# Kernel optimization log

Measured on AMD Instinct MI355X. Metric: run time of the kernel, lower is better.

## Reference

```python
import jax, jax.numpy as jnp
import numpy as np
from jax import lax


def setup_inputs() -> dict:
    key = jax.random.key(0)
    ks = jax.random.split(key, 6)
    B, S, I, H = 64, 2048, 512, 512
    stdv = 1.0 / np.sqrt(H)
    return {
        "inputs": jax.random.normal(ks[0], (B, S, I), dtype=jnp.float32),
        "state": jax.random.normal(ks[1], (B, H), dtype=jnp.float32),
        "w_ih": jax.random.uniform(ks[2], (H, I), minval=-stdv, maxval=stdv, dtype=jnp.float32),
        "b_ih": jax.random.uniform(ks[3], (H, 1), minval=-stdv, maxval=stdv, dtype=jnp.float32),
        "w_hh": jax.random.uniform(ks[4], (H, H), minval=-stdv, maxval=stdv, dtype=jnp.float32),
        "b_hh": jax.random.uniform(ks[5], (H, 1), minval=-stdv, maxval=stdv, dtype=jnp.float32),
    }


def reference(inputs, state, w_ih, b_ih, w_hh, b_hh):
    """Tanh RNN: h_t = tanh(W_ih x_t + b_ih + W_hh h_{t-1} + b_hh).
    Returns (hidden_seq [S*B, H] (per-step states concatenated along dim 0,
    matching torch.cat(dim=0) in the original), h_last_T [H, B])."""
    B, S, I = inputs.shape
    H = w_hh.shape[0]
    # Hoist the input projection out of the recurrence: [B, S, H]
    x_proj = jnp.einsum('bsi,hi->bsh', inputs, w_ih) + (b_ih[:, 0] + b_hh[:, 0])

    def step(h, xp_t):  # h: [B, H], xp_t: [B, H]
        h_new = jnp.tanh(xp_t + h @ w_hh.T)
        return h_new, h_new

    h_last, hs = lax.scan(step, state, jnp.swapaxes(x_proj, 0, 1))  # hs: [S, B, H]
    hidden_seq = hs.reshape(S * B, H)
    return hidden_seq, h_last.T  # h_last.T matches the original's returned h_t of shape [H, B]
```

## Files before the change

kernel.cpp:

```cpp
#include <hip/hip_runtime.h>


typedef _Float16 half8 __attribute__((ext_vector_type(8)));
typedef _Float16 half4 __attribute__((ext_vector_type(4)));
typedef float f32x4 __attribute__((ext_vector_type(4)));
typedef unsigned long long u64;

#define S_SZ 2048
#define OUT1_OFF 67108864ull

#define XP_OFF    0ull
#define WHH_OFF   134217728ull
#define WIH_OFF   134742016ull
#define BIAS_OFF  135266304ull

#define WLDS_SZ   131072
#define HB_SZ     8192
#define SMEM_SZ   147456

__device__ __forceinline__ float fast_tanh(float x) {
    float a = exp2f(x * 2.8853900817779268f);
    return (a - 1.0f) * __builtin_amdgcn_rcpf(a + 1.0f);
}

__global__ void prep_kernel(const float* __restrict__ wih, const float* __restrict__ whh,
                            const float* __restrict__ bih, const float* __restrict__ bhh,
                            _Float16* __restrict__ wih16, _Float16* __restrict__ whh16,
                            float* __restrict__ bias)
{
    const int i = blockIdx.x * 256 + threadIdx.x;
    wih16[i] = (_Float16)wih[i];
    whh16[i] = (_Float16)whh[i];
    if (i < 512) bias[i] = bih[i] + bhh[i];
}

__global__ __launch_bounds__(512, 1) void xproj_kernel(
    const float* __restrict__ inputs, const _Float16* __restrict__ wih16,
    const float* __restrict__ bias, _Float16* __restrict__ xp16)
{
    __shared__ _Float16 Alds[64 * 512];
    const int s = blockIdx.x;

    for (int idx = threadIdx.x; idx < 64 * 128; idx += 512) {
        const int row = idx >> 7, chunk = idx & 127;
        const float4 v = *reinterpret_cast<const float4*>(
            inputs + ((size_t)row * S_SZ + s) * 512 + chunk * 4);
        half4 hv;
        hv[0] = (_Float16)v.x; hv[1] = (_Float16)v.y;
        hv[2] = (_Float16)v.z; hv[3] = (_Float16)v.w;
        const int bc = (chunk * 8) ^ ((row & 7) << 4);
        *reinterpret_cast<half4*>(reinterpret_cast<char*>(Alds) + row * 1024 + bc) = hv;
    }
    __syncthreads();

    const int lane = threadIdx.x & 63, w = threadIdx.x >> 6;
    const int l15 = lane & 15, lg = lane >> 4;

    f32x4 acc[4][4];
    #pragma unroll
    for (int m = 0; m < 4; ++m)
        #pragma unroll
        for (int n = 0; n < 4; ++n)
            acc[m][n] = 0.0f;

    for (int kk = 0; kk < 16; ++kk) {
        half8 af[4], bf[4];
        #pragma unroll
        for (int m = 0; m < 4; ++m) {
            const int row = m * 16 + l15;
            const int bc = (kk * 64 + lg * 16) ^ ((row & 7) << 4);
            af[m] = *reinterpret_cast<const half8*>(
                reinterpret_cast<const char*>(Alds) + row * 1024 + bc);
        }
        #pragma unroll
        for (int n = 0; n < 4; ++n) {
            const int col = w * 64 + n * 16 + l15;
            bf[n] = *reinterpret_cast<const half8*>(wih16 + (size_t)col * 512 + kk * 32 + lg * 8);
        }
        #pragma unroll
        for (int m = 0; m < 4; ++m)
            #pragma unroll
            for (int n = 0; n < 4; ++n)
                acc[m][n] = __builtin_amdgcn_mfma_f32_16x16x32_f16(bf[n], af[m], acc[m][n], 0, 0, 0);
    }

    #pragma unroll
    for (int m = 0; m < 4; ++m) {
        const int brow = m * 16 + l15;
        #pragma unroll
        for (int n = 0; n < 4; ++n) {
            const int j0 = w * 64 + n * 16 + lg * 4;
            const float4 bv = *reinterpret_cast<const float4*>(bias + j0);
            half4 hv;
            hv[0] = (_Float16)(acc[m][n][0] + bv.x);
            hv[1] = (_Float16)(acc[m][n][1] + bv.y);
            hv[2] = (_Float16)(acc[m][n][2] + bv.z);
            hv[3] = (_Float16)(acc[m][n][3] + bv.w);
            *reinterpret_cast<half4*>(xp16 + ((size_t)s * 64 + brow) * 512 + j0) = hv;
        }
    }
}

__global__ __launch_bounds__(256, 1) void rnn_step_kernel(
    const _Float16* __restrict__ whh16, const _Float16* __restrict__ xp16,
    const float* __restrict__ state, float* __restrict__ out)
{
    extern __shared__ __align__(16) char smem[];
    char* wlds = smem;
    char* hb   = smem + WLDS_SZ;

    const int r = blockIdx.x;
    const int tid = threadIdx.x;
    const int lane = tid & 63, w = tid >> 6;
    const int l15 = lane & 15, lg = lane >> 4;
    const int row8 = l15 & 7;
    const bool hi = (l15 >= 8);

    for (int idx = tid; idx < 16 * 512; idx += 256) {
        const int c = idx >> 9, jj = idx & 511;
        const int kk = 12 + (c >> 2), lgc = c & 3;
        *reinterpret_cast<half8*>(wlds + c * 8192 + jj * 16) =
            *reinterpret_cast<const half8*>(whh16 + (size_t)jj * 512 + kk * 32 + lgc * 8);
    }
    for (int idx = tid; idx < 512; idx += 256) {
        const int row = idx & 7, lgc = (idx >> 3) & 3, kk = idx >> 5;
        const float* sp = state + (size_t)(r * 8 + row) * 512 + kk * 32 + lgc * 8;
        const float4 v0 = *reinterpret_cast<const float4*>(sp);
        const float4 v1 = *reinterpret_cast<const float4*>(sp + 4);
        half8 hv;
        hv[0] = (_Float16)v0.x; hv[1] = (_Float16)v0.y;
        hv[2] = (_Float16)v0.z; hv[3] = (_Float16)v0.w;
        hv[4] = (_Float16)v1.x; hv[5] = (_Float16)v1.y;
        hv[6] = (_Float16)v1.z; hv[7] = (_Float16)v1.w;
        *reinterpret_cast<half8*>(hb + ((kk * 4 + lgc) * 8 + row) * 16) = hv;
    }

    half8 wa[64], wv[32];
    {
        const _Float16* wp = whh16 + (size_t)(w * 128 + l15) * 512 + lg * 8;
        #pragma unroll
        for (int jt = 0; jt < 8; ++jt) {
            #pragma unroll
            for (int kk = 0; kk < 8; ++kk)
                wa[jt * 8 + kk] = *reinterpret_cast<const half8*>(wp + jt * 16 * 512 + kk * 32);
            #pragma unroll
            for (int kk = 8; kk < 12; ++kk)
                wv[jt * 4 + kk - 8] = *reinterpret_cast<const half8*>(wp + jt * 16 * 512 + kk * 32);
        }
    }
    #pragma unroll
    for (int i = 0; i < 64; ++i) asm volatile("" : "+a"(wa[i]));
    #pragma unroll
    for (int i = 0; i < 32; ++i) asm volatile("" : "+v"(wv[i]));

    u64 xq[4];
    {
        const _Float16* xpb = xp16 + (size_t)(r * 8 + row8) * 512
                              + w * 128 + (hi ? 64 : 0) + lg * 4;
        #pragma unroll
        for (int i = 0; i < 4; ++i)
            xq[i] = *reinterpret_cast<const u64*>(xpb + i * 16);
    }

    __syncthreads();

    #pragma unroll 1
    for (int t = 0; t < S_SZ; ++t) {
        const char* hc = hb + (t & 1) * HB_SZ;
        char* hn = hb + ((t + 1) & 1) * HB_SZ;

        f32x4 acc[8];
        #pragma unroll
        for (int jt = 0; jt < 8; ++jt) acc[jt] = 0.0f;

        #pragma unroll
        for (int kk = 0; kk < 8; ++kk) {
            const half8 bf = *reinterpret_cast<const half8*>(
                hc + ((kk * 4 + lg) * 8 + row8) * 16);
            #pragma unroll
            for (int jt = 0; jt < 8; ++jt)
                acc[jt] = __builtin_amdgcn_mfma_f32_16x16x32_f16(
                    wa[jt * 8 + kk], bf, acc[jt], 0, 0, 0);
        }
        #pragma unroll
        for (int kk = 8; kk < 12; ++kk) {
            const half8 bf = *reinterpret_cast<const half8*>(
                hc + ((kk * 4 + lg) * 8 + row8) * 16);
            #pragma unroll
            for (int jt = 0; jt < 8; ++jt)
                acc[jt] = __builtin_amdgcn_mfma_f32_16x16x32_f16(
                    wv[jt * 4 + kk - 8], bf, acc[jt], 0, 0, 0);
        }
        #pragma unroll
        for (int kk = 12; kk < 16; ++kk) {
            const half8 bf = *reinterpret_cast<const half8*>(
                hc + ((kk * 4 + lg) * 8 + row8) * 16);
            const char* wc = wlds + ((kk - 12) * 4 + lg) * 8192;
            #pragma unroll
            for (int jt = 0; jt < 8; ++jt) {
                const half8 a = *reinterpret_cast<const half8*>(
                    wc + (w * 128 + jt * 16 + l15) * 16);
                acc[jt] = __builtin_amdgcn_mfma_f32_16x16x32_f16(a, bf, acc[jt], 0, 0, 0);
            }
        }

        const int rowi = r * 8 + row8;
        #pragma unroll
        for (int i = 0; i < 4; ++i) {
            const f32x4 a = hi ? acc[i + 4] : acc[i];
            union { _Float16 h[4]; u64 u; } xv, hp;
            xv.u = xq[i];
            f32x4 f;
            #pragma unroll
            for (int q = 0; q < 4; ++q) {
                f[q] = fast_tanh(a[q] + (float)xv.h[q]);
                hp.h[q] = (_Float16)f[q];
            }
            const int j0 = w * 128 + (hi ? 64 : 0) + i * 16 + lg * 4;
            const int e = (((j0 >> 5) * 4 + ((j0 >> 3) & 3)) * 8 + row8);
            *reinterpret_cast<u64*>(hn + e * 16 + (lg & 1) * 8) = hp.u;
            *reinterpret_cast<f32x4*>(out + ((size_t)t * 64 + rowi) * 512 + j0) = f;
            if (t == S_SZ - 1) {
                #pragma unroll
                for (int q = 0; q < 4; ++q)
                    out[OUT1_OFF + (size_t)(j0 + q) * 64 + rowi] = f[q];
            }
        }

        if (t + 1 < S_SZ) {
            const _Float16* xpb = xp16 + ((size_t)(t + 1) * 64 + rowi) * 512
                                  + w * 128 + (hi ? 64 : 0) + lg * 4;
            #pragma unroll
            for (int i = 0; i < 4; ++i)
                xq[i] = *reinterpret_cast<const u64*>(xpb + i * 16);
        }

        asm volatile("s_waitcnt lgkmcnt(0)" ::: "memory");
        __builtin_amdgcn_s_barrier();
    }
}

extern "C" void kernel_launch(void* const* d_in, const int* in_sizes, int n_in,
                              void* d_out, int out_size, void* d_ws, size_t ws_size,
                              hipStream_t stream)
{
    const float* inputs = (const float*)d_in[0];
    const float* state  = (const float*)d_in[1];
    const float* w_ih   = (const float*)d_in[2];
    const float* b_ih   = (const float*)d_in[3];
    const float* w_hh   = (const float*)d_in[4];
    const float* b_hh   = (const float*)d_in[5];
    float* out = (float*)d_out;
    char* ws = (char*)d_ws;

    _Float16* xp16  = (_Float16*)(ws + XP_OFF);
    _Float16* whh16 = (_Float16*)(ws + WHH_OFF);
    _Float16* wih16 = (_Float16*)(ws + WIH_OFF);
    float*    bias  = (float*)(ws + BIAS_OFF);

    hipFuncSetAttribute((const void*)rnn_step_kernel,
                        hipFuncAttributeMaxDynamicSharedMemorySize, SMEM_SZ);

    prep_kernel<<<1024, 256, 0, stream>>>(w_ih, w_hh, b_ih, b_hh, wih16, whh16, bias);
    xproj_kernel<<<S_SZ, 512, 0, stream>>>(inputs, wih16, bias, xp16);
    rnn_step_kernel<<<8, 256, SMEM_SZ, stream>>>(whh16, xp16, state, out);
}
```

Before: 6.852 ms.

## Split recurrent step across eight waves per block instead of four

Doubles the threads per recurrence block from 256 to 512. Each wave now owns 64 hidden columns instead of 128, which halves the per-wave MFMA chain, the register-resident weight slice and the epilogue work on every serial step. The register-resident weights are merged into a single AGPR array, and the h write offset is recomputed to match the new column mapping. In exchange there are more waves to synchronise at each step's barrier, and the launch bound of two blocks per CU does not match the 144KB LDS each block uses.

Result: slower. 8.523 ms (+24.4%).

```diff
diff --git a/kernel.cpp b/kernel.cpp
--- a/kernel.cpp
+++ b/kernel.cpp
@@ -101,7 +101,7 @@
     }
 }
 
-__global__ __launch_bounds__(256, 1) void rnn_step_kernel(
+__global__ __launch_bounds__(512, 2) void rnn_step_kernel(
     const _Float16* __restrict__ whh16, const _Float16* __restrict__ xp16,
     const float* __restrict__ state, float* __restrict__ out)
 {
@@ -116,13 +116,14 @@
     const int row8 = l15 & 7;
     const bool hi = (l15 >= 8);
 
-    for (int idx = tid; idx < 16 * 512; idx += 256) {
+    for (int idx = tid; idx < 16 * 512; idx += 512) {
         const int c = idx >> 9, jj = idx & 511;
         const int kk = 12 + (c >> 2), lgc = c & 3;
         *reinterpret_cast<half8*>(wlds + c * 8192 + jj * 16) =
             *reinterpret_cast<const half8*>(whh16 + (size_t)jj * 512 + kk * 32 + lgc * 8);
     }
-    for (int idx = tid; idx < 512; idx += 256) {
+    if (tid < 512) {
+        const int idx = tid;
         const int row = idx & 7, lgc = (idx >> 3) & 3, kk = idx >> 5;
         const float* sp = state + (size_t)(r * 8 + row) * 512 + kk * 32 + lgc * 8;
         const float4 v0 = *reinterpret_cast<const float4*>(sp);
@@ -135,31 +136,24 @@
         *reinterpret_cast<half8*>(hb + ((kk * 4 + lgc) * 8 + row) * 16) = hv;
     }
 
-    half8 wa[64], wv[32];
+    half8 wa[48];
     {
-        const _Float16* wp = whh16 + (size_t)(w * 128 + l15) * 512 + lg * 8;
-        #pragma unroll
-        for (int jt = 0; jt < 8; ++jt) {
-            #pragma unroll
-            for (int kk = 0; kk < 8; ++kk)
-                wa[jt * 8 + kk] = *reinterpret_cast<const half8*>(wp + jt * 16 * 512 + kk * 32);
-            #pragma unroll
-            for (int kk = 8; kk < 12; ++kk)
-                wv[jt * 4 + kk - 8] = *reinterpret_cast<const half8*>(wp + jt * 16 * 512 + kk * 32);
-        }
+        const _Float16* wp = whh16 + (size_t)(w * 64 + l15) * 512 + lg * 8;
+        #pragma unroll
+        for (int jt = 0; jt < 4; ++jt)
+            #pragma unroll
+            for (int kk = 0; kk < 12; ++kk)
+                wa[jt * 12 + kk] = *reinterpret_cast<const half8*>(wp + jt * 16 * 512 + kk * 32);
     }
     #pragma unroll
-    for (int i = 0; i < 64; ++i) asm volatile("" : "+a"(wa[i]));
-    #pragma unroll
-    for (int i = 0; i < 32; ++i) asm volatile("" : "+v"(wv[i]));
-
-    u64 xq[4];
+    for (int i = 0; i < 48; ++i) asm volatile("" : "+a"(wa[i]));
+
+    u64 xq[2];
     {
         const _Float16* xpb = xp16 + (size_t)(r * 8 + row8) * 512
-                              + w * 128 + (hi ? 64 : 0) + lg * 4;
-        #pragma unroll
-        for (int i = 0; i < 4; ++i)
-            xq[i] = *reinterpret_cast<const u64*>(xpb + i * 16);
+                              + w * 64 + (hi ? 32 : 0) + lg * 4;
+        xq[0] = *reinterpret_cast<const u64*>(xpb);
+        xq[1] = *reinterpret_cast<const u64*>(xpb + 16);
     }
 
     __syncthreads();
@@ -169,27 +163,18 @@
         const char* hc = hb + (t & 1) * HB_SZ;
         char* hn = hb + ((t + 1) & 1) * HB_SZ;
 
-        f32x4 acc[8];
-        #pragma unroll
-        for (int jt = 0; jt < 8; ++jt) acc[jt] = 0.0f;
-
-        #pragma unroll
-        for (int kk = 0; kk < 8; ++kk) {
+        f32x4 acc[4];
+        #pragma unroll
+        for (int jt = 0; jt < 4; ++jt) acc[jt] = 0.0f;
+
+        #pragma unroll
+        for (int kk = 0; kk < 12; ++kk) {
             const half8 bf = *reinterpret_cast<const half8*>(
                 hc + ((kk * 4 + lg) * 8 + row8) * 16);
             #pragma unroll
-            for (int jt = 0; jt < 8; ++jt)
+            for (int jt = 0; jt < 4; ++jt)
                 acc[jt] = __builtin_amdgcn_mfma_f32_16x16x32_f16(
-                    wa[jt * 8 + kk], bf, acc[jt], 0, 0, 0);
-        }
-        #pragma unroll
-        for (int kk = 8; kk < 12; ++kk) {
-            const half8 bf = *reinterpret_cast<const half8*>(
-                hc + ((kk * 4 + lg) * 8 + row8) * 16);
-            #pragma unroll
-            for (int jt = 0; jt < 8; ++jt)
-                acc[jt] = __builtin_amdgcn_mfma_f32_16x16x32_f16(
-                    wv[jt * 4 + kk - 8], bf, acc[jt], 0, 0, 0);
+                    wa[jt * 12 + kk], bf, acc[jt], 0, 0, 0);
         }
         #pragma unroll
         for (int kk = 12; kk < 16; ++kk) {
@@ -197,17 +182,17 @@
                 hc + ((kk * 4 + lg) * 8 + row8) * 16);
             const char* wc = wlds + ((kk - 12) * 4 + lg) * 8192;
             #pragma unroll
-            for (int jt = 0; jt < 8; ++jt) {
+            for (int jt = 0; jt < 4; ++jt) {
                 const half8 a = *reinterpret_cast<const half8*>(
-                    wc + (w * 128 + jt * 16 + l15) * 16);
+                    wc + (w * 64 + jt * 16 + l15) * 16);
                 acc[jt] = __builtin_amdgcn_mfma_f32_16x16x32_f16(a, bf, acc[jt], 0, 0, 0);
             }
         }
 
         const int rowi = r * 8 + row8;
         #pragma unroll
-        for (int i = 0; i < 4; ++i) {
-            const f32x4 a = hi ? acc[i + 4] : acc[i];
+        for (int i = 0; i < 2; ++i) {
+            const f32x4 a = hi ? acc[i + 2] : acc[i];
             union { _Float16 h[4]; u64 u; } xv, hp;
             xv.u = xq[i];
             f32x4 f;
@@ -216,9 +201,9 @@
                 f[q] = fast_tanh(a[q] + (float)xv.h[q]);
                 hp.h[q] = (_Float16)f[q];
             }
-            const int j0 = w * 128 + (hi ? 64 : 0) + i * 16 + lg * 4;
+            const int j0 = w * 64 + (hi ? 32 : 0) + i * 16 + lg * 4;
             const int e = (((j0 >> 5) * 4 + ((j0 >> 3) & 3)) * 8 + row8);
-            *reinterpret_cast<u64*>(hn + e * 16 + (lg & 1) * 8) = hp.u;
+            *reinterpret_cast<u64*>(hn + e * 16 + ((j0 >> 2) & 1) * 8) = hp.u;
             *reinterpret_cast<f32x4*>(out + ((size_t)t * 64 + rowi) * 512 + j0) = f;
             if (t == S_SZ - 1) {
                 #pragma unroll
@@ -229,10 +214,9 @@
 
         if (t + 1 < S_SZ) {
             const _Float16* xpb = xp16 + ((size_t)(t + 1) * 64 + rowi) * 512
-                                  + w * 128 + (hi ? 64 : 0) + lg * 4;
-            #pragma unroll
-            for (int i = 0; i < 4; ++i)
-                xq[i] = *reinterpret_cast<const u64*>(xpb + i * 16);
+                                  + w * 64 + (hi ? 32 : 0) + lg * 4;
+            xq[0] = *reinterpret_cast<const u64*>(xpb);
+            xq[1] = *reinterpret_cast<const u64*>(xpb + 16);
         }
 
         asm volatile("s_waitcnt lgkmcnt(0)" ::: "memory");
@@ -263,5 +247,5 @@
 
     prep_kernel<<<1024, 256, 0, stream>>>(w_ih, w_hh, b_ih, b_hh, wih16, whh16, bias);
     xproj_kernel<<<S_SZ, 512, 0, stream>>>(inputs, wih16, bias, xp16);
-    rnn_step_kernel<<<8, 256, SMEM_SZ, stream>>>(whh16, xp16, state, out);
-}
+    rnn_step_kernel<<<8, 512, SMEM_SZ, stream>>>(whh16, xp16, state, out);
+}
```
